# Kernel tuning notes

Measured on AMD Instinct MI355X. Metric: run time of the kernel, lower is better.

The kernel has to match this reference:

```python
import jax, jax.numpy as jnp
import numpy as np

N = 50000
E = 1600000
IN_FEATS = 256
HIDDEN = 32
HEADS = 4
NUM_CLASSES = 16
NEG_SLOPE = 0.2  # DGL GATConv default leaky_relu slope


def gat_conv(x, src, dst, W, b, attn_l, attn_r, n_nodes):
    """DGL-style GATConv. x:[N,Fin], W:[Fin,H*D], attn_l/attn_r:[H,D], b:[H*D].
    Returns [N, H, D]."""
    H, D = attn_l.shape
    feat = (x @ W).reshape(-1, H, D)                     # [N,H,D]
    el = jnp.sum(feat * attn_l, axis=-1)                 # [N,H]
    er = jnp.sum(feat * attn_r, axis=-1)                 # [N,H]
    e = jax.nn.leaky_relu(el[src] + er[dst], NEG_SLOPE)  # [E,H]
    # segment softmax over incoming edges of each dst node
    m = jax.ops.segment_max(e, dst, num_segments=n_nodes)
    m = jnp.where(jnp.isfinite(m), m, 0.0)               # empty segments -> -inf
    ex = jnp.exp(e - m[dst])                             # [E,H]
    denom = jax.ops.segment_sum(ex, dst, num_segments=n_nodes)
    alpha = ex / jnp.maximum(denom, 1e-9)[dst]           # [E,H]
    msg = feat[src] * alpha[:, :, None]                  # [E,H,D]
    out = jax.ops.segment_sum(msg, dst, num_segments=n_nodes)
    return out + b.reshape(H, D)


def setup_inputs() -> dict:
    key = jax.random.key(0)
    ks = jax.random.split(key, 12)
    x = jax.random.normal(ks[0], (N, IN_FEATS), dtype=jnp.float32)
    src = jax.random.randint(ks[1], (E,), 0, N, dtype=jnp.int32)
    dst = jax.random.randint(ks[2], (E,), 0, N, dtype=jnp.int32)
    s1 = 1.0 / np.sqrt(IN_FEATS)
    W1 = jax.random.normal(ks[3], (IN_FEATS, HEADS * HIDDEN), dtype=jnp.float32) * s1
    b1 = jnp.zeros((HEADS * HIDDEN,), dtype=jnp.float32)
    al1 = jax.random.normal(ks[4], (HEADS, HIDDEN), dtype=jnp.float32) * 0.1
    ar1 = jax.random.normal(ks[5], (HEADS, HIDDEN), dtype=jnp.float32) * 0.1
    F2 = HEADS * HIDDEN
    s2 = 1.0 / np.sqrt(F2)
    W2 = jax.random.normal(ks[6], (F2, NUM_CLASSES), dtype=jnp.float32) * s2
    b2 = jnp.zeros((NUM_CLASSES,), dtype=jnp.float32)
    al2 = jax.random.normal(ks[7], (1, NUM_CLASSES), dtype=jnp.float32) * 0.1
    ar2 = jax.random.normal(ks[8], (1, NUM_CLASSES), dtype=jnp.float32) * 0.1
    return {"x": x, "src": src, "dst": dst,
            "W1": W1, "b1": b1, "al1": al1, "ar1": ar1,
            "W2": W2, "b2": b2, "al2": al2, "ar2": ar2}


def reference(x, src, dst, W1, b1, al1, ar1, W2, b2, al2, ar2):
    h = jax.nn.elu(gat_conv(x, src, dst, W1, b1, al1, ar1, N))  # [N,H,D]
    h = h.reshape(N, HEADS * HIDDEN)                            # flatten(1)
    out = gat_conv(h, src, dst, W2, b2, al2, ar2, N)            # [N,1,C]
    return out.mean(axis=1)                                     # [N,C]
```

## Files before the change

kernel.cpp:

```cpp
#include <hip/hip_runtime.h>
#include <hip/hip_fp16.h>

#define N_NODES 50000
#define N_EDGES 1600000
#define FIN 256
#define HD 128
#define NHEADS 4
#define C2 16
#define NEG 0.2f

#define EBLK 4096
#define NBLK 391
#define NBUCK 391
#define BSH 7
#define BMASK 127
#define MAXB 5120

__device__ __forceinline__ float elu1(float x) { return x > 0.f ? x : __expf(x) - 1.f; }
__device__ __forceinline__ float lexp(float e) { return __expf(e > 0.f ? e : NEG * e); }


__global__ __launch_bounds__(256) void k_bhist(const int* __restrict__ dst,
                                               int* __restrict__ ghist) {
    __shared__ int lh[NBUCK];
    int tid = threadIdx.x, b = blockIdx.x;
    for (int t = tid; t < NBUCK; t += 256) lh[t] = 0;
    __syncthreads();
    int base = b * EBLK;
    int nq = (min(EBLK, N_EDGES - base)) >> 2;
    const int4* d4 = (const int4*)(dst + base);
    for (int q = tid; q < nq; q += 256) {
        int4 d = d4[q];
        atomicAdd(&lh[d.x >> BSH], 1);
        atomicAdd(&lh[d.y >> BSH], 1);
        atomicAdd(&lh[d.z >> BSH], 1);
        atomicAdd(&lh[d.w >> BSH], 1);
    }
    __syncthreads();
    for (int t = tid; t < NBUCK; t += 256) ghist[t * NBLK + b] = lh[t];
}

__global__ __launch_bounds__(256) void k_bscan1(int* __restrict__ ghist,
                                                int* __restrict__ bucket_tot) {
    __shared__ int s[256];
    int B = blockIdx.x, t = threadIdx.x;
    int* row = ghist + (size_t)B * NBLK;
    int i0 = 2 * t, i1 = 2 * t + 1;
    int a0 = (i0 < NBLK) ? row[i0] : 0;
    int a1 = (i1 < NBLK) ? row[i1] : 0;
    int pair = a0 + a1;
    s[t] = pair;
    __syncthreads();
    for (int off = 1; off < 256; off <<= 1) {
        int u = (t >= off) ? s[t - off] : 0;
        __syncthreads();
        s[t] += u;
        __syncthreads();
    }
    int excl = s[t] - pair;
    if (i0 < NBLK) row[i0] = excl;
    if (i1 < NBLK) row[i1] = excl + a0;
    if (t == 255) bucket_tot[B] = s[255];
}

__global__ __launch_bounds__(512) void k_bscan2(const int* __restrict__ bucket_tot,
                                                int* __restrict__ bucket_base,
                                                int* __restrict__ rowstart) {
    __shared__ int s[512];
    int t = threadIdx.x;
    int v = (t < NBUCK) ? bucket_tot[t] : 0;
    s[t] = v;
    __syncthreads();
    for (int off = 1; off < 512; off <<= 1) {
        int u = (t >= off) ? s[t - off] : 0;
        __syncthreads();
        s[t] += u;
        __syncthreads();
    }
    if (t < NBUCK) bucket_base[t] = s[t] - v;
    if (t == 0) { bucket_base[NBUCK] = N_EDGES; rowstart[N_NODES] = N_EDGES; }
}

__global__ __launch_bounds__(256) void k_bscatter(
        const int* __restrict__ src, const int* __restrict__ dst,
        const int* __restrict__ ghist, const int* __restrict__ bucket_base,
        int* __restrict__ ebuf) {
    __shared__ int lcur[NBUCK];
    int tid = threadIdx.x, b = blockIdx.x;
    for (int t = tid; t < NBUCK; t += 256)
        lcur[t] = bucket_base[t] + ghist[t * NBLK + b];
    __syncthreads();
    int base = b * EBLK;
    int nq = (min(EBLK, N_EDGES - base)) >> 2;
    const int4* s4 = (const int4*)(src + base);
    const int4* d4 = (const int4*)(dst + base);
    for (int q = tid; q < nq; q += 256) {
        int4 s = s4[q];
        int4 d = d4[q];
        int p;
        p = atomicAdd(&lcur[d.x >> BSH], 1); ebuf[p] = (s.x << BSH) | (d.x & BMASK);
        p = atomicAdd(&lcur[d.y >> BSH], 1); ebuf[p] = (s.y << BSH) | (d.y & BMASK);
        p = atomicAdd(&lcur[d.z >> BSH], 1); ebuf[p] = (s.z << BSH) | (d.z & BMASK);
        p = atomicAdd(&lcur[d.w >> BSH], 1); ebuf[p] = (s.w << BSH) | (d.w & BMASK);
    }
}

__global__ __launch_bounds__(256) void k_bsort(
        const int* __restrict__ ebuf, const int* __restrict__ bucket_base,
        int* __restrict__ sorted_src, int* __restrict__ rowstart) {
    __shared__ int ein[MAXB];
    __shared__ int eout[MAXB];
    __shared__ int hist[128];
    __shared__ int sc[128];
    __shared__ int cursor[128];
    int tid = threadIdx.x, B = blockIdx.x;
    int base = bucket_base[B];
    int n = bucket_base[B + 1] - base;
    if (tid < 128) hist[tid] = 0;
    __syncthreads();
    for (int i = tid; i < n; i += 256) {
        int v = ebuf[base + i];
        ein[i] = v;
        atomicAdd(&hist[v & BMASK], 1);
    }
    __syncthreads();
    if (tid < 128) sc[tid] = hist[tid];
    __syncthreads();
    for (int off = 1; off < 128; off <<= 1) {
        int u = 0;
        if (tid < 128 && tid >= off) u = sc[tid - off];
        __syncthreads();
        if (tid < 128) sc[tid] += u;
        __syncthreads();
    }
    if (tid < 128) {
        int ex = sc[tid] - hist[tid];
        cursor[tid] = ex;
        int node = B * 128 + tid;
        if (node < N_NODES) rowstart[node] = base + ex;
    }
    __syncthreads();
    for (int i = tid; i < n; i += 256) {
        int v = ein[i];
        int p = atomicAdd(&cursor[v & BMASK], 1);
        eout[p] = v >> BSH;
    }
    __syncthreads();
    for (int i = tid; i < n; i += 256) sorted_src[base + i] = eout[i];
}


__global__ __launch_bounds__(256) void k_gemm1(
        const float* __restrict__ x, const float* __restrict__ W1,
        const float* __restrict__ al1, const float* __restrict__ ar1,
        __half* __restrict__ feat1h, float* __restrict__ el1, float* __restrict__ er1) {
    __shared__ float xs[16 * 64];
    __shared__ float ws[16 * 128];
    int tid = threadIdx.x;
    int nb = blockIdx.x * 64;
    int ct = tid & 15;
    int nt = tid >> 4;

    float acc[4][8];
    #pragma unroll
    for (int n = 0; n < 4; n++)
        #pragma unroll
        for (int c = 0; c < 8; c++) acc[n][c] = 0.f;

    int lnode = tid & 63;
    int kg = tid >> 6;
    int gnode = nb + lnode; if (gnode >= N_NODES) gnode = N_NODES - 1;
    const float4* xrow = (const float4*)(x + (size_t)gnode * FIN);
    const float4* W14 = (const float4*)W1;

    for (int k0 = 0; k0 < FIN; k0 += 16) {
        float4 a0 = xrow[(k0 >> 2) + kg];
        float4 w0 = W14[(size_t)k0 * 32 + tid];
        float4 w1 = W14[(size_t)k0 * 32 + tid + 256];
        __syncthreads();
        int kb = kg * 4;
        xs[(kb + 0) * 64 + lnode] = a0.x;
        xs[(kb + 1) * 64 + lnode] = a0.y;
        xs[(kb + 2) * 64 + lnode] = a0.z;
        xs[(kb + 3) * 64 + lnode] = a0.w;
        ((float4*)ws)[tid] = w0;
        ((float4*)ws)[tid + 256] = w1;
        __syncthreads();
        #pragma unroll
        for (int kk = 0; kk < 16; kk++) {
            float4 xa = ((const float4*)xs)[kk * 16 + nt];
            float4 wa = ((const float4*)ws)[kk * 32 + ct];
            float4 wb = ((const float4*)ws)[kk * 32 + 16 + ct];
            float xn[4] = {xa.x, xa.y, xa.z, xa.w};
            float wc[8] = {wa.x, wa.y, wa.z, wa.w, wb.x, wb.y, wb.z, wb.w};
            #pragma unroll
            for (int n = 0; n < 4; n++)
                #pragma unroll
                for (int c = 0; c < 8; c++)
                    acc[n][c] += xn[n] * wc[c];
        }
    }

    float alvA[4], arvA[4], alvB[4], arvB[4];
    #pragma unroll
    for (int j = 0; j < 4; j++) {
        alvA[j] = al1[4 * ct + j];      arvA[j] = ar1[4 * ct + j];
        alvB[j] = al1[64 + 4 * ct + j]; arvB[j] = ar1[64 + 4 * ct + j];
    }
    int headA = ct >> 3;
    int headB = 2 + (ct >> 3);
    #pragma unroll
    for (int n = 0; n < 4; n++) {
        int node = nb + nt * 4 + n;
        bool ok = node < N_NODES;
        if (ok) {
            __half2 ha[2], hb[2];
            ha[0] = __floats2half2_rn(acc[n][0], acc[n][1]);
            ha[1] = __floats2half2_rn(acc[n][2], acc[n][3]);
            hb[0] = __floats2half2_rn(acc[n][4], acc[n][5]);
            hb[1] = __floats2half2_rn(acc[n][6], acc[n][7]);
            *(float2*)(feat1h + (size_t)node * HD + 4 * ct) = *(float2*)ha;
            *(float2*)(feat1h + (size_t)node * HD + 64 + 4 * ct) = *(float2*)hb;
        }
        float plA = 0.f, prA = 0.f, plB = 0.f, prB = 0.f;
        #pragma unroll
        for (int j = 0; j < 4; j++) {
            plA += acc[n][j] * alvA[j];     prA += acc[n][j] * arvA[j];
            plB += acc[n][4 + j] * alvB[j]; prB += acc[n][4 + j] * arvB[j];
        }
        #pragma unroll
        for (int m = 1; m <= 4; m <<= 1) {
            plA += __shfl_xor(plA, m); prA += __shfl_xor(prA, m);
            plB += __shfl_xor(plB, m); prB += __shfl_xor(prB, m);
        }
        if (ok && (ct & 7) == 0) {
            el1[node * 4 + headA] = plA; er1[node * 4 + headA] = prA;
            el1[node * 4 + headB] = plB; er1[node * 4 + headB] = prB;
        }
    }
}


__global__ __launch_bounds__(256) void k_agg1(
        const int* __restrict__ rowstart, const int* __restrict__ sorted_src,
        const float* __restrict__ el1, const float* __restrict__ er1,
        const __half* __restrict__ feat1h, const float* __restrict__ b1,
        float* __restrict__ h) {
    int tid = threadIdx.x;
    int d = blockIdx.x * 4 + (tid >> 6);
    int lane = tid & 63;
    int eg = lane >> 4;
    int cl = lane & 15;
    int head = cl >> 2;
    float er = er1[d * 4 + head];
    int start = rowstart[d], end = rowstart[d + 1];
    float acc[8];
    #pragma unroll
    for (int k = 0; k < 8; k++) acc[k] = 0.f;
    float wsum = 0.f;

    for (int i = start; i < end; i += 8) {
        int e0 = i + eg, e1 = i + 4 + eg;
        bool ok0 = e0 < end, ok1 = e1 < end;
        int e0c = ok0 ? e0 : end - 1;
        int e1c = ok1 ? e1 : end - 1;
        int s0 = sorted_src[e0c];
        int s1 = sorted_src[e1c];
        float el0v = el1[s0 * 4 + head];
        float el1v = el1[s1 * 4 + head];
        float4 r0 = *(const float4*)(feat1h + (size_t)s0 * HD + cl * 8);
        float4 r1 = *(const float4*)(feat1h + (size_t)s1 * HD + cl * 8);
        float w0 = ok0 ? lexp(el0v + er) : 0.f;
        float w1 = ok1 ? lexp(el1v + er) : 0.f;
        const __half2* p0 = (const __half2*)&r0;
        const __half2* p1 = (const __half2*)&r1;
        #pragma unroll
        for (int q = 0; q < 4; q++) {
            float2 f0 = __half22float2(p0[q]);
            float2 f1 = __half22float2(p1[q]);
            acc[2 * q]     += w0 * f0.x + w1 * f1.x;
            acc[2 * q + 1] += w0 * f0.y + w1 * f1.y;
        }
        wsum += w0 + w1;
    }
    #pragma unroll
    for (int k = 0; k < 8; k++) {
        acc[k] += __shfl_xor(acc[k], 16);
        acc[k] += __shfl_xor(acc[k], 32);
    }
    wsum += __shfl_xor(wsum, 16);
    wsum += __shfl_xor(wsum, 32);
    if (eg == 0) {
        float inv = 1.f / fmaxf(wsum, 1e-9f);
        float v[8];
        #pragma unroll
        for (int k = 0; k < 8; k++) v[k] = elu1(acc[k] * inv + b1[cl * 8 + k]);
        float4* hp = (float4*)(h + (size_t)d * HD + cl * 8);
        hp[0] = make_float4(v[0], v[1], v[2], v[3]);
        hp[1] = make_float4(v[4], v[5], v[6], v[7]);
    }
}


__global__ __launch_bounds__(256) void k_gemm2(
        const float* __restrict__ h, const float* __restrict__ W2,
        const float* __restrict__ al2, const float* __restrict__ ar2,
        float* __restrict__ feat2, float* __restrict__ el2, float* __restrict__ er2) {
    __shared__ float hs[16 * 132];
    __shared__ float w2t[16 * 132];
    int tid = threadIdx.x;
    int nb = blockIdx.x * 16;
    for (int idx = tid; idx < 512; idx += 256) {
        int row = idx >> 5, kk = idx & 31;
        ((float4*)(hs + row * 132))[kk] = ((const float4*)h)[(size_t)(nb + row) * 32 + kk];
    }
    for (int idx = tid; idx < 2048; idx += 256) {
        int k = idx >> 4, c = idx & 15;
        w2t[c * 132 + k] = W2[idx];
    }
    __syncthreads();
    int nl = tid >> 4, col = tid & 15;
    const float4* hv = (const float4*)(hs + nl * 132);
    const float4* wv = (const float4*)(w2t + col * 132);
    float acc = 0.f;
    #pragma unroll
    for (int kk = 0; kk < 32; kk++) {
        float4 a = hv[kk], w = wv[kk];
        acc += a.x * w.x + a.y * w.y + a.z * w.z + a.w * w.w;
    }
    int node = nb + nl;
    feat2[node * 16 + col] = acc;
    float pl = acc * al2[col], pr = acc * ar2[col];
    #pragma unroll
    for (int m = 8; m >= 1; m >>= 1) {
        pl += __shfl_xor(pl, m);
        pr += __shfl_xor(pr, m);
    }
    if (col == 0) { el2[node] = pl; er2[node] = pr; }
}


__global__ __launch_bounds__(256) void k_agg2(
        const int* __restrict__ rowstart, const int* __restrict__ sorted_src,
        const float* __restrict__ el2, const float* __restrict__ er2,
        const float* __restrict__ feat2, const float* __restrict__ b2,
        float* __restrict__ out) {
    int tid = threadIdx.x;
    int d = blockIdx.x * 4 + (tid >> 6);
    int lane = tid & 63;
    int eg = lane >> 2;
    int cq = lane & 3;
    float er = er2[d];
    int start = rowstart[d], end = rowstart[d + 1];
    float4 acc = make_float4(0.f, 0.f, 0.f, 0.f);
    float wsum = 0.f;
    for (int i = start; i < end; i += 16) {
        int e = i + eg;
        bool ok = e < end;
        int ec = ok ? e : end - 1;
        int s = sorted_src[ec];
        float elv = el2[s];
        float4 f = ((const float4*)feat2)[(size_t)s * 4 + cq];
        float ev = elv + er;
        float wr = __expf(ev > 0.f ? ev : NEG * ev);
        float w = ok ? wr : 0.f;
        acc.x += w * f.x; acc.y += w * f.y; acc.z += w * f.z; acc.w += w * f.w;
        wsum += w;
    }
    #pragma unroll
    for (int m = 4; m <= 32; m <<= 1) {
        acc.x += __shfl_xor(acc.x, m);
        acc.y += __shfl_xor(acc.y, m);
        acc.z += __shfl_xor(acc.z, m);
        acc.w += __shfl_xor(acc.w, m);
        wsum  += __shfl_xor(wsum, m);
    }
    if (lane < 4) {
        float inv = 1.f / fmaxf(wsum, 1e-9f);
        float4 bv = ((const float4*)b2)[cq];
        float4 o = make_float4(acc.x * inv + bv.x, acc.y * inv + bv.y,
                               acc.z * inv + bv.z, acc.w * inv + bv.w);
        ((float4*)out)[(size_t)d * 4 + cq] = o;
    }
}


extern "C" void kernel_launch(void* const* d_in, const int* in_sizes, int n_in,
                              void* d_out, int out_size, void* d_ws, size_t ws_size,
                              hipStream_t stream) {
    const float* x   = (const float*)d_in[0];
    const int*   src = (const int*)d_in[1];
    const int*   dst = (const int*)d_in[2];
    const float* W1  = (const float*)d_in[3];
    const float* b1  = (const float*)d_in[4];
    const float* al1 = (const float*)d_in[5];
    const float* ar1 = (const float*)d_in[6];
    const float* W2  = (const float*)d_in[7];
    const float* b2  = (const float*)d_in[8];
    const float* al2 = (const float*)d_in[9];
    const float* ar2 = (const float*)d_in[10];
    float* out = (float*)d_out;

    char* ws = (char*)d_ws;
    size_t off = 0;
    auto alloc = [&](size_t bytes) -> char* {
        char* p = ws + off;
        off += (bytes + 255) & ~(size_t)255;
        return p;
    };
    __half* feat1h    = (__half*)alloc((size_t)N_NODES * HD * 2);
    float* h          = (float*)alloc((size_t)N_NODES * HD * 4);
    float* el1        = (float*)alloc((size_t)N_NODES * 4 * 4);
    float* er1        = (float*)alloc((size_t)N_NODES * 4 * 4);
    float* feat2      = (float*)alloc((size_t)N_NODES * C2 * 4);
    float* el2        = (float*)alloc((size_t)N_NODES * 4);
    float* er2        = (float*)alloc((size_t)N_NODES * 4);
    int*   ghist      = (int*)alloc((size_t)NBUCK * NBLK * 4);
    int*   bucket_tot = (int*)alloc((size_t)NBUCK * 4);
    int*   bucket_base= (int*)alloc((size_t)(NBUCK + 1) * 4);
    int*   rowstart   = (int*)alloc((size_t)(N_NODES + 1) * 4);
    int*   ebuf       = (int*)alloc((size_t)N_EDGES * 4);
    int*   sorted_src = (int*)alloc((size_t)N_EDGES * 4);

    k_bhist<<<NBLK, 256, 0, stream>>>(dst, ghist);
    k_bscan1<<<NBUCK, 256, 0, stream>>>(ghist, bucket_tot);
    k_bscan2<<<1, 512, 0, stream>>>(bucket_tot, bucket_base, rowstart);
    k_bscatter<<<NBLK, 256, 0, stream>>>(src, dst, ghist, bucket_base, ebuf);
    k_bsort<<<NBUCK, 256, 0, stream>>>(ebuf, bucket_base, sorted_src, rowstart);
    k_gemm1<<<(N_NODES + 63) / 64, 256, 0, stream>>>(x, W1, al1, ar1, feat1h, el1, er1);
    k_agg1<<<N_NODES / 4, 256, 0, stream>>>(rowstart, sorted_src, el1, er1, feat1h, b1, h);
    k_gemm2<<<N_NODES / 16, 256, 0, stream>>>(h, W2, al2, ar2, feat2, el2, er2);
    k_agg2<<<N_NODES / 4, 256, 0, stream>>>(rowstart, sorted_src, el2, er2, feat2, b2, out);
}
```

Before: 274.2 us.

## Compute first GAT projection GEMM with fp16 MFMA instead of FP32 FMA

Rewrites the first-layer projection GEMM to use 16x16x32 fp16 MFMA instructions, with x converted to fp16 while staging and W1 pre-transposed to fp16 by a new small kernel. Shared-memory tiles use an XOR swizzle and global loads for the next K step are register-prefetched. This replaces the scalar FP32 FMA loop, which is compute-bound, at the cost of fp16 rounding of inputs and one extra kernel launch.

```diff
diff --git a/kernel.cpp b/kernel.cpp
--- a/kernel.cpp
+++ b/kernel.cpp
@@ -15,6 +15,10 @@
 #define BSH 7
 #define BMASK 127
 #define MAXB 5120
+
+typedef _Float16 v8h __attribute__((ext_vector_type(8)));
+typedef float v4f __attribute__((ext_vector_type(4)));
+union F4H8 { float4 f; v8h h; };
 
 __device__ __forceinline__ float elu1(float x) { return x > 0.f ? x : __expf(x) - 1.f; }
 __device__ __forceinline__ float lexp(float e) { return __expf(e > 0.f ? e : NEG * e); }
@@ -150,92 +154,117 @@
 }
 
 
+__global__ __launch_bounds__(256) void k_w1half(const float* __restrict__ W1,
+                                                _Float16* __restrict__ W1T) {
+    int idx = blockIdx.x * 256 + threadIdx.x;
+    int k = idx >> 7, c = idx & 127;
+    W1T[c * 256 + k] = (_Float16)W1[idx];
+}
+
+
 __global__ __launch_bounds__(256) void k_gemm1(
-        const float* __restrict__ x, const float* __restrict__ W1,
+        const float* __restrict__ x, const _Float16* __restrict__ W1T,
         const float* __restrict__ al1, const float* __restrict__ ar1,
         __half* __restrict__ feat1h, float* __restrict__ el1, float* __restrict__ er1) {
-    __shared__ float xs[16 * 64];
-    __shared__ float ws[16 * 128];
+    __shared__ v8h As[64 * 4];
+    __shared__ v8h Bs[128 * 4];
     int tid = threadIdx.x;
     int nb = blockIdx.x * 64;
-    int ct = tid & 15;
-    int nt = tid >> 4;
-
-    float acc[4][8];
-    #pragma unroll
-    for (int n = 0; n < 4; n++)
-        #pragma unroll
-        for (int c = 0; c < 8; c++) acc[n][c] = 0.f;
-
-    int lnode = tid & 63;
-    int kg = tid >> 6;
-    int gnode = nb + lnode; if (gnode >= N_NODES) gnode = N_NODES - 1;
+    int wid = tid >> 6, lane = tid & 63;
+    int wm = wid & 1, wn = wid >> 1;
+    int q = lane >> 4, lm = lane & 15;
+
+    int anode = tid >> 2, ach = tid & 3;
+    int gnode = nb + anode; if (gnode >= N_NODES) gnode = N_NODES - 1;
     const float4* xrow = (const float4*)(x + (size_t)gnode * FIN);
-    const float4* W14 = (const float4*)W1;
-
-    for (int k0 = 0; k0 < FIN; k0 += 16) {
-        float4 a0 = xrow[(k0 >> 2) + kg];
-        float4 w0 = W14[(size_t)k0 * 32 + tid];
-        float4 w1 = W14[(size_t)k0 * 32 + tid + 256];
-        __syncthreads();
-        int kb = kg * 4;
-        xs[(kb + 0) * 64 + lnode] = a0.x;
-        xs[(kb + 1) * 64 + lnode] = a0.y;
-        xs[(kb + 2) * 64 + lnode] = a0.z;
-        xs[(kb + 3) * 64 + lnode] = a0.w;
-        ((float4*)ws)[tid] = w0;
-        ((float4*)ws)[tid + 256] = w1;
-        __syncthreads();
-        #pragma unroll
-        for (int kk = 0; kk < 16; kk++) {
-            float4 xa = ((const float4*)xs)[kk * 16 + nt];
-            float4 wa = ((const float4*)ws)[kk * 32 + ct];
-            float4 wb = ((const float4*)ws)[kk * 32 + 16 + ct];
-            float xn[4] = {xa.x, xa.y, xa.z, xa.w};
-            float wc[8] = {wa.x, wa.y, wa.z, wa.w, wb.x, wb.y, wb.z, wb.w};
+    int bc = tid >> 2, bch = tid & 3;
+
+    v4f acc[2][4];
+    #pragma unroll
+    for (int mt = 0; mt < 2; mt++)
+        #pragma unroll
+        for (int nt = 0; nt < 4; nt++) acc[mt][nt] = (v4f)(0.f);
+
+    float4 xa0 = xrow[ach * 2];
+    float4 xa1 = xrow[ach * 2 + 1];
+    F4H8 wb0, wb1;
+    wb0.f = *(const float4*)(W1T + bc * 256 + bch * 8);
+    wb1.f = *(const float4*)(W1T + (bc + 64) * 256 + bch * 8);
+
+    for (int step = 0; step < 8; step++) {
+        __syncthreads();
+        {
+            v8h av;
+            av[0] = (_Float16)xa0.x; av[1] = (_Float16)xa0.y;
+            av[2] = (_Float16)xa0.z; av[3] = (_Float16)xa0.w;
+            av[4] = (_Float16)xa1.x; av[5] = (_Float16)xa1.y;
+            av[6] = (_Float16)xa1.z; av[7] = (_Float16)xa1.w;
+            As[anode * 4 + (ach ^ (anode & 3))] = av;
+            Bs[bc * 4 + (bch ^ (bc & 3))] = wb0.h;
+            Bs[(bc + 64) * 4 + (bch ^ (bc & 3))] = wb1.h;
+        }
+        __syncthreads();
+        if (step < 7) {
+            int k0 = (step + 1) * 32;
+            xa0 = xrow[(k0 >> 2) + ach * 2];
+            xa1 = xrow[(k0 >> 2) + ach * 2 + 1];
+            wb0.f = *(const float4*)(W1T + bc * 256 + k0 + bch * 8);
+            wb1.f = *(const float4*)(W1T + (bc + 64) * 256 + k0 + bch * 8);
+        }
+        v8h af[2], bf[4];
+        #pragma unroll
+        for (int mt = 0; mt < 2; mt++) {
+            int nl = wm * 32 + mt * 16 + lm;
+            af[mt] = As[nl * 4 + (q ^ (nl & 3))];
+        }
+        #pragma unroll
+        for (int nt = 0; nt < 4; nt++) {
+            int cl = wn * 64 + nt * 16 + lm;
+            bf[nt] = Bs[cl * 4 + (q ^ (cl & 3))];
+        }
+        #pragma unroll
+        for (int mt = 0; mt < 2; mt++)
             #pragma unroll
-            for (int n = 0; n < 4; n++)
-                #pragma unroll
-                for (int c = 0; c < 8; c++)
-                    acc[n][c] += xn[n] * wc[c];
-        }
-    }
-
-    float alvA[4], arvA[4], alvB[4], arvB[4];
-    #pragma unroll
-    for (int j = 0; j < 4; j++) {
-        alvA[j] = al1[4 * ct + j];      arvA[j] = ar1[4 * ct + j];
-        alvB[j] = al1[64 + 4 * ct + j]; arvB[j] = ar1[64 + 4 * ct + j];
-    }
-    int headA = ct >> 3;
-    int headB = 2 + (ct >> 3);
-    #pragma unroll
-    for (int n = 0; n < 4; n++) {
-        int node = nb + nt * 4 + n;
-        bool ok = node < N_NODES;
-        if (ok) {
-            __half2 ha[2], hb[2];
-            ha[0] = __floats2half2_rn(acc[n][0], acc[n][1]);
-            ha[1] = __floats2half2_rn(acc[n][2], acc[n][3]);
-            hb[0] = __floats2half2_rn(acc[n][4], acc[n][5]);
-            hb[1] = __floats2half2_rn(acc[n][6], acc[n][7]);
-            *(float2*)(feat1h + (size_t)node * HD + 4 * ct) = *(float2*)ha;
-            *(float2*)(feat1h + (size_t)node * HD + 64 + 4 * ct) = *(float2*)hb;
-        }
-        float plA = 0.f, prA = 0.f, plB = 0.f, prB = 0.f;
-        #pragma unroll
-        for (int j = 0; j < 4; j++) {
-            plA += acc[n][j] * alvA[j];     prA += acc[n][j] * arvA[j];
-            plB += acc[n][4 + j] * alvB[j]; prB += acc[n][4 + j] * arvB[j];
-        }
-        #pragma unroll
-        for (int m = 1; m <= 4; m <<= 1) {
-            plA += __shfl_xor(plA, m); prA += __shfl_xor(prA, m);
-            plB += __shfl_xor(plB, m); prB += __shfl_xor(prB, m);
-        }
-        if (ok && (ct & 7) == 0) {
-            el1[node * 4 + headA] = plA; er1[node * 4 + headA] = prA;
-            el1[node * 4 + headB] = plB; er1[node * 4 + headB] = prB;
+            for (int nt = 0; nt < 4; nt++)
+                acc[mt][nt] = __builtin_amdgcn_mfma_f32_16x16x32_f16(
+                    af[mt], bf[nt], acc[mt][nt], 0, 0, 0);
+    }
+
+    float alv[4], arv[4];
+    #pragma unroll
+    for (int nt = 0; nt < 4; nt++) {
+        alv[nt] = al1[wn * 64 + nt * 16 + lm];
+        arv[nt] = ar1[wn * 64 + nt * 16 + lm];
+    }
+    int h0 = 2 * wn, h1 = 2 * wn + 1;
+    #pragma unroll
+    for (int mt = 0; mt < 2; mt++) {
+        #pragma unroll
+        for (int r = 0; r < 4; r++) {
+            int node = nb + wm * 32 + mt * 16 + q * 4 + r;
+            bool ok = node < N_NODES;
+            float v0 = acc[mt][0][r], v1 = acc[mt][1][r];
+            float v2 = acc[mt][2][r], v3 = acc[mt][3][r];
+            if (ok) {
+                __half* fp = feat1h + (size_t)node * HD + wn * 64 + lm;
+                fp[0]  = __float2half(v0);
+                fp[16] = __float2half(v1);
+                fp[32] = __float2half(v2);
+                fp[48] = __float2half(v3);
+            }
+            float pl0 = v0 * alv[0] + v1 * alv[1];
+            float pr0 = v0 * arv[0] + v1 * arv[1];
+            float pl1 = v2 * alv[2] + v3 * alv[3];
+            float pr1 = v2 * arv[2] + v3 * arv[3];
+            #pragma unroll
+            for (int m = 1; m <= 8; m <<= 1) {
+                pl0 += __shfl_xor(pl0, m); pr0 += __shfl_xor(pr0, m);
+                pl1 += __shfl_xor(pl1, m); pr1 += __shfl_xor(pr1, m);
+            }
+            if (ok && lm == 0) {
+                el1[node * 4 + h0] = pl0; er1[node * 4 + h0] = pr0;
+                el1[node * 4 + h1] = pl1; er1[node * 4 + h1] = pr1;
+            }
         }
     }
 }
@@ -408,26 +437,28 @@
         off += (bytes + 255) & ~(size_t)255;
         return p;
     };
-    __half* feat1h    = (__half*)alloc((size_t)N_NODES * HD * 2);
-    float* h          = (float*)alloc((size_t)N_NODES * HD * 4);
-    float* el1        = (float*)alloc((size_t)N_NODES * 4 * 4);
-    float* er1        = (float*)alloc((size_t)N_NODES * 4 * 4);
-    float* feat2      = (float*)alloc((size_t)N_NODES * C2 * 4);
-    float* el2        = (float*)alloc((size_t)N_NODES * 4);
-    float* er2        = (float*)alloc((size_t)N_NODES * 4);
-    int*   ghist      = (int*)alloc((size_t)NBUCK * NBLK * 4);
-    int*   bucket_tot = (int*)alloc((size_t)NBUCK * 4);
-    int*   bucket_base= (int*)alloc((size_t)(NBUCK + 1) * 4);
-    int*   rowstart   = (int*)alloc((size_t)(N_NODES + 1) * 4);
-    int*   ebuf       = (int*)alloc((size_t)N_EDGES * 4);
-    int*   sorted_src = (int*)alloc((size_t)N_EDGES * 4);
+    __half* feat1h     = (__half*)alloc((size_t)N_NODES * HD * 2);
+    _Float16* W1T      = (_Float16*)alloc((size_t)FIN * HD * 2);
+    float* h           = (float*)alloc((size_t)N_NODES * HD * 4);
+    float* el1         = (float*)alloc((size_t)N_NODES * 4 * 4);
+    float* er1         = (float*)alloc((size_t)N_NODES * 4 * 4);
+    float* feat2       = (float*)alloc((size_t)N_NODES * C2 * 4);
+    float* el2         = (float*)alloc((size_t)N_NODES * 4);
+    float* er2         = (float*)alloc((size_t)N_NODES * 4);
+    int*   ghist       = (int*)alloc((size_t)NBUCK * NBLK * 4);
+    int*   bucket_tot  = (int*)alloc((size_t)NBUCK * 4);
+    int*   bucket_base = (int*)alloc((size_t)(NBUCK + 1) * 4);
+    int*   rowstart    = (int*)alloc((size_t)(N_NODES + 1) * 4);
+    int*   ebuf        = (int*)alloc((size_t)N_EDGES * 4);
+    int*   sorted_src  = (int*)alloc((size_t)N_EDGES * 4);
 
     k_bhist<<<NBLK, 256, 0, stream>>>(dst, ghist);
     k_bscan1<<<NBUCK, 256, 0, stream>>>(ghist, bucket_tot);
     k_bscan2<<<1, 512, 0, stream>>>(bucket_tot, bucket_base, rowstart);
     k_bscatter<<<NBLK, 256, 0, stream>>>(src, dst, ghist, bucket_base, ebuf);
     k_bsort<<<NBUCK, 256, 0, stream>>>(ebuf, bucket_base, sorted_src, rowstart);
-    k_gemm1<<<(N_NODES + 63) / 64, 256, 0, stream>>>(x, W1, al1, ar1, feat1h, el1, er1);
+    k_w1half<<<128, 256, 0, stream>>>(W1, W1T);
+    k_gemm1<<<(N_NODES + 63) / 64, 256, 0, stream>>>(x, W1T, al1, ar1, feat1h, el1, er1);
     k_agg1<<<N_NODES / 4, 256, 0, stream>>>(rowstart, sorted_src, el1, er1, feat1h, b1, h);
     k_gemm2<<<N_NODES / 16, 256, 0, stream>>>(h, W2, al2, ar2, feat2, el2, er2);
     k_agg2<<<N_NODES / 4, 256, 0, stream>>>(rowstart, sorted_src, el2, er2, feat2, b2, out);
```

Measured after the change: 245.9 us. 10.3% less time.
